# Optimization experiments

Measured on AMD Instinct MI355X. Metric: run time of the kernel, lower is better.

## Reference

```python
import math
import jax, jax.numpy as jnp
import numpy as np

NUM_HEADS = 8
C_HIDDEN = 32
C_Q = 64
C_KV = 64
INF = 1.0e9


def setup_inputs() -> dict:
    key = jax.random.key(0)
    ks = jax.random.split(key, 8)
    B, S, Q, KV = 1, 128, 256, 256
    H, D = NUM_HEADS, C_HIDDEN
    input_q = jax.random.normal(ks[0], (B, S, Q, C_Q), dtype=jnp.float32)
    input_kv = jax.random.normal(ks[1], (B, S, KV, C_KV), dtype=jnp.float32)
    mask = jnp.ones((B, S, 1, 1, KV), dtype=jnp.float32)
    bias = jax.random.normal(ks[2], (B, 1, H, Q, KV), dtype=jnp.float32)
    # Glorot-ish init for projections
    wq = jax.random.normal(ks[3], (C_Q, H * D), dtype=jnp.float32) * (1.0 / math.sqrt(C_Q))
    wk = jax.random.normal(ks[4], (C_KV, H * D), dtype=jnp.float32) * (1.0 / math.sqrt(C_KV))
    wv = jax.random.normal(ks[5], (C_KV, H * D), dtype=jnp.float32) * (1.0 / math.sqrt(C_KV))
    wo = jax.random.normal(ks[6], (H * D, C_Q), dtype=jnp.float32) * (1.0 / math.sqrt(H * D))
    bo = jnp.zeros((C_Q,), dtype=jnp.float32)
    return {"input_q": input_q, "input_kv": input_kv, "mask": mask, "bias": bias,
            "wq": wq, "wk": wk, "wv": wv, "wo": wo, "bo": bo}


def _split_heads(x):
    # [..., L, H*D] -> [..., H, L, D]
    *lead, L, HD = x.shape
    x = x.reshape(*lead, L, NUM_HEADS, C_HIDDEN)
    return jnp.swapaxes(x, -2, -3)


def reference(input_q, input_kv, mask, bias, wq, wk, wv, wo, bo):
    q = _split_heads(input_q @ wq)   # [B,S,H,Q,D]
    k = _split_heads(input_kv @ wk)  # [B,S,H,KV,D]
    v = _split_heads(input_kv @ wv)  # [B,S,H,KV,D]
    scaling = 1.0 / math.sqrt(C_HIDDEN)
    a = jnp.einsum("bshqd,bshkd->bshqk", q * scaling, k)
    a = a + (mask - 1.0) * INF + bias
    a = jax.nn.softmax(a, axis=-1)
    o = jnp.einsum("bshqk,bshkd->bshqd", a, v)
    o = jnp.swapaxes(o, -2, -3)  # [B,S,Q,H,D]
    o = o.reshape(o.shape[:-2] + (NUM_HEADS * C_HIDDEN,))
    return o @ wo + bo
```

## Files before the change

### kernel.cpp

```cpp
#include <hip/hip_runtime.h>

typedef __bf16 bf16_t;
typedef __bf16 bf16x4_t __attribute__((ext_vector_type(4)));
typedef __bf16 bf16x8 __attribute__((ext_vector_type(8)));
typedef float f32x4 __attribute__((ext_vector_type(4)));

#define NH 8
#define DH 32
#define QL 256
#define KL 256
#define CIN 64
#define HD 256

__device__ __forceinline__ bf16_t f2bf(float x) { return (bf16_t)x; }

__device__ __forceinline__ f32x4 mfma16(bf16x8 a, bf16x8 b, f32x4 c) {
    return __builtin_amdgcn_mfma_f32_16x16x32_bf16(a, b, c, 0, 0, 0);
}

__device__ __forceinline__ float exp2_raw(float x) {
    float r;
    asm("v_exp_f32 %0, %1" : "=v"(r) : "v"(x));
    return r;
}

__launch_bounds__(256)
__global__ void pack_w(const float* __restrict__ Wq, const float* __restrict__ Wk,
                       const float* __restrict__ Wv, const float* __restrict__ Wo,
                       bf16_t* __restrict__ WqF, bf16_t* __restrict__ WkF,
                       bf16_t* __restrict__ WvF, bf16_t* __restrict__ WoF) {
    const int h = blockIdx.x;
    const int tid = threadIdx.x, lane = tid & 63, w = tid >> 6;
    const int quad = lane >> 4, l16 = lane & 15;
    if (w < 3) {
        const float* __restrict__ W = (w == 0) ? Wq : (w == 1 ? Wk : Wv);
        bf16_t* __restrict__ F = (w == 0) ? WqF : (w == 1 ? WkF : WvF);
#pragma unroll
        for (int nt = 0; nt < 2; ++nt)
#pragma unroll
            for (int ks = 0; ks < 2; ++ks) {
                bf16x8 f;
#pragma unroll
                for (int j = 0; j < 8; ++j)
                    f[j] = f2bf(W[(ks * 32 + quad * 8 + j) * HD + h * DH + nt * 16 + l16]);
                *(bf16x8*)&F[(size_t)((h * 4 + nt * 2 + ks) * 512) + lane * 8] = f;
            }
    } else {
#pragma unroll
        for (int nt = 0; nt < 4; ++nt) {
            bf16x8 f;
#pragma unroll
            for (int j = 0; j < 8; ++j)
                f[j] = f2bf(Wo[(h * DH + (j >> 2) * 16 + quad * 4 + (j & 3)) * CIN +
                               nt * 16 + l16]);
            *(bf16x8*)&WoF[(size_t)((h * 4 + nt) * 512) + lane * 8] = f;
        }
    }
}

__launch_bounds__(256, 2)
__global__ void fused_pipe5(const float* __restrict__ Xq, const float* __restrict__ Xkv,
                            const float* __restrict__ Mask, const float* __restrict__ Bias,
                            const bf16_t* __restrict__ WqF, const bf16_t* __restrict__ WkF,
                            const bf16_t* __restrict__ WvF, const bf16_t* __restrict__ WoF,
                            const float* __restrict__ Bo, float* __restrict__ Out) {
    const int b = blockIdx.x;
    const int s = b & 127, qq = b >> 7;
    const int tid = threadIdx.x, lane = tid & 63, w = tid >> 6;
    const int quad = lane >> 4, l16 = lane & 15;
    const int tg = qq * 4 + w;
    const f32x4 vzero = {0.f, 0.f, 0.f, 0.f};
    constexpr float L2E = 1.4426950408889634f;

    __shared__ __attribute__((aligned(16))) bf16_t sK[2][KL * 40];
    __shared__ __attribute__((aligned(16))) bf16_t sVT[2][DH][264];
    __shared__ __attribute__((aligned(16))) float sMask[KL];

    if (tid < 64) {
        const f32x4 m4 = *(const f32x4*)&Mask[s * KL + tid * 4];
        f32x4 mm;
#pragma unroll
        for (int j = 0; j < 4; ++j) mm[j] = (m4[j] - 1.0f) * (1.0e9f * L2E);
        *(f32x4*)&sMask[tid * 4] = mm;
    }

    bf16x8 xk[4][2];
#pragma unroll
    for (int t = 0; t < 4; ++t) {
        const int row = (w * 4 + t) * 16 + l16;
        const float* src = &Xkv[(size_t)(s * QL + row) * CIN];
#pragma unroll
        for (int ks = 0; ks < 2; ++ks) {
            const f32x4 lo = *(const f32x4*)&src[ks * 32 + quad * 8];
            const f32x4 hi = *(const f32x4*)&src[ks * 32 + quad * 8 + 4];
            bf16x8 f;
#pragma unroll
            for (int j = 0; j < 4; ++j) { f[j] = f2bf(lo[j]); f[4 + j] = f2bf(hi[j]); }
            xk[t][ks] = f;
        }
    }
    bf16x8 xq[2];
    {
        const int row = tg * 16 + l16;
        const float* src = &Xq[(size_t)(s * QL + row) * CIN];
        const float qs = 0.17677669529663687f * L2E;
#pragma unroll
        for (int ks = 0; ks < 2; ++ks) {
            const f32x4 lo = *(const f32x4*)&src[ks * 32 + quad * 8];
            const f32x4 hi = *(const f32x4*)&src[ks * 32 + quad * 8 + 4];
            bf16x8 f;
#pragma unroll
            for (int j = 0; j < 4; ++j) {
                f[j] = f2bf(lo[j] * qs);
                f[4 + j] = f2bf(hi[j] * qs);
            }
            xq[ks] = f;
        }
    }

    auto projKV = [&](int h, int buf) {
        bf16x8 bk[2][2], bv[2][2];
#pragma unroll
        for (int nt = 0; nt < 2; ++nt)
#pragma unroll
            for (int ks = 0; ks < 2; ++ks) {
                bk[nt][ks] = *(const bf16x8*)&WkF[(size_t)((h * 4 + nt * 2 + ks) * 512) + lane * 8];
                bv[nt][ks] = *(const bf16x8*)&WvF[(size_t)((h * 4 + nt * 2 + ks) * 512) + lane * 8];
            }
#pragma unroll
        for (int t = 0; t < 4; ++t) {
            const int row = (w * 4 + t) * 16 + l16;
#pragma unroll
            for (int nt = 0; nt < 2; ++nt) {
                f32x4 c = mfma16(bk[nt][0], xk[t][0], vzero);
                c = mfma16(bk[nt][1], xk[t][1], c);
                bf16x4_t p4;
#pragma unroll
                for (int r = 0; r < 4; ++r) p4[r] = f2bf(c[r]);
                *(bf16x4_t*)&sK[buf][row * 40 + quad * 8 + nt * 4] = p4;
            }
        }
#pragma unroll
        for (int t = 0; t < 4; ++t) {
            const int c0 = (w * 4 + t) * 16 + quad * 4;
#pragma unroll
            for (int nt = 0; nt < 2; ++nt) {
                f32x4 c = mfma16(xk[t][0], bv[nt][0], vzero);
                c = mfma16(xk[t][1], bv[nt][1], c);
                bf16x4_t p4;
#pragma unroll
                for (int r = 0; r < 4; ++r) p4[r] = f2bf(c[r]);
                *(bf16x4_t*)&sVT[buf][nt * 16 + l16][c0] = p4;
            }
        }
    };
    auto projQ = [&](int h) -> bf16x8 {
        bf16x8 bq[2][2];
#pragma unroll
        for (int nt = 0; nt < 2; ++nt)
#pragma unroll
            for (int ks = 0; ks < 2; ++ks)
                bq[nt][ks] = *(const bf16x8*)&WqF[(size_t)((h * 4 + nt * 2 + ks) * 512) + lane * 8];
        bf16x8 q;
#pragma unroll
        for (int nt = 0; nt < 2; ++nt) {
            f32x4 c = mfma16(bq[nt][0], xq[0], vzero);
            c = mfma16(bq[nt][1], xq[1], c);
#pragma unroll
            for (int r = 0; r < 4; ++r) q[nt * 4 + r] = f2bf(c[r]);
        }
        return q;
    };

    auto loadVA = [&](int p, int c, bf16x8& v0, bf16x8& v1) {
        const bf16x4_t a00 = *(const bf16x4_t*)&sVT[p][l16][c * 32 + quad * 4];
        const bf16x4_t a01 = *(const bf16x4_t*)&sVT[p][l16][c * 32 + 16 + quad * 4];
        const bf16x4_t a10 = *(const bf16x4_t*)&sVT[p][16 + l16][c * 32 + quad * 4];
        const bf16x4_t a11 = *(const bf16x4_t*)&sVT[p][16 + l16][c * 32 + 16 + quad * 4];
#pragma unroll
        for (int j = 0; j < 4; ++j) {
            v0[j] = a00[j];
            v0[4 + j] = a01[j];
            v1[j] = a10[j];
            v1[4 + j] = a11[j];
        }
    };

    f32x4 acc[4];
#pragma unroll
    for (int nt = 0; nt < 4; ++nt) acc[nt] = vzero;

    f32x4 sv[16];
    {
        const float* bb = &Bias[(size_t)(tg * 16 + l16) * KL];
#pragma unroll
        for (int ct = 0; ct < 16; ++ct) sv[ct] = *(const f32x4*)&bb[ct * 16 + quad * 4];
    }
    projKV(0, 0);
    bf16x8 qfr = projQ(0);
    __syncthreads();
#pragma unroll
    for (int ct = 0; ct < 16; ++ct) {
        const f32x4 m4 = *(const f32x4*)&sMask[ct * 16 + quad * 4];
#pragma unroll
        for (int r = 0; r < 4; ++r) sv[ct][r] = sv[ct][r] * L2E + m4[r];
    }

#pragma unroll 1
    for (int h = 0; h < NH; ++h) {
        const int p = h & 1;
        const int hn = (h + 1) & 7;
        const float* bbn = &Bias[(size_t)(hn * QL + tg * 16 + l16) * KL];

#pragma unroll
        for (int ct = 0; ct < 16; ++ct) {
            const bf16x8 ak = *(const bf16x8*)&sK[p][(ct * 16 + l16) * 40 + quad * 8];
            sv[ct] = mfma16(ak, qfr, sv[ct]);
        }

        if (h + 1 < NH) projKV(h + 1, p ^ 1);

        bf16x8 bwo[4];
#pragma unroll
        for (int nt = 0; nt < 4; ++nt)
            bwo[nt] = *(const bf16x8*)&WoF[(size_t)((h * 4 + nt) * 512) + lane * 8];

        bf16x8 vc0, vc1;
        loadVA(p, 0, vc0, vc1);

        f32x4 vmx = sv[0];
#pragma unroll
        for (int ct = 1; ct < 16; ++ct)
#pragma unroll
            for (int r = 0; r < 4; ++r) vmx[r] = fmaxf(vmx[r], sv[ct][r]);
        float mx = fmaxf(fmaxf(vmx[0], vmx[1]), fmaxf(vmx[2], vmx[3]));
        mx = fmaxf(mx, __shfl_xor(mx, 16, 64));
        mx = fmaxf(mx, __shfl_xor(mx, 32, 64));
        f32x4 vsum = vzero;
#pragma unroll
        for (int ct = 0; ct < 16; ++ct)
#pragma unroll
            for (int r = 0; r < 4; ++r) {
                const float e = exp2_raw(sv[ct][r] - mx);
                sv[ct][r] = e;
                vsum[r] += e;
            }
        float sum = (vsum[0] + vsum[1]) + (vsum[2] + vsum[3]);
        sum += __shfl_xor(sum, 16, 64);
        sum += __shfl_xor(sum, 32, 64);
        const float rs = 1.0f / sum;

        f32x4 ot0 = vzero, ot1 = vzero;
#pragma unroll
        for (int c = 0; c < 8; ++c) {
            bf16x8 vn0, vn1;
            if (c < 7) loadVA(p, c + 1, vn0, vn1);
            bf16x8 pf;
#pragma unroll
            for (int j = 0; j < 4; ++j) {
                pf[j] = f2bf(sv[2 * c][j]);
                pf[4 + j] = f2bf(sv[2 * c + 1][j]);
            }
            sv[2 * c] = *(const f32x4*)&bbn[(2 * c) * 16 + quad * 4];
            sv[2 * c + 1] = *(const f32x4*)&bbn[(2 * c + 1) * 16 + quad * 4];
            ot0 = mfma16(vc0, pf, ot0);
            ot1 = mfma16(vc1, pf, ot1);
            vc0 = vn0;
            vc1 = vn1;
        }

        {
            bf16x8 af;
#pragma unroll
            for (int r = 0; r < 4; ++r) {
                af[r] = f2bf(ot0[r] * rs);
                af[4 + r] = f2bf(ot1[r] * rs);
            }
#pragma unroll
            for (int nt = 0; nt < 4; ++nt) acc[nt] = mfma16(af, bwo[nt], acc[nt]);
        }

        if (h + 1 < NH) {
            qfr = projQ(h + 1);
#pragma unroll
            for (int ct = 0; ct < 16; ++ct) {
                const f32x4 m4 = *(const f32x4*)&sMask[ct * 16 + quad * 4];
#pragma unroll
                for (int r = 0; r < 4; ++r) sv[ct][r] = sv[ct][r] * L2E + m4[r];
            }
        }

        __syncthreads();
    }

    const int orow = s * QL + tg * 16 + quad * 4;
#pragma unroll
    for (int nt = 0; nt < 4; ++nt) {
        const float bo = Bo[nt * 16 + l16];
#pragma unroll
        for (int r = 0; r < 4; ++r)
            Out[(size_t)(orow + r) * CIN + nt * 16 + l16] = acc[nt][r] + bo;
    }
}

extern "C" void kernel_launch(void* const* d_in, const int* in_sizes, int n_in,
                              void* d_out, int out_size, void* d_ws, size_t ws_size,
                              hipStream_t stream) {
    const float* Xq   = (const float*)d_in[0];
    const float* Xkv  = (const float*)d_in[1];
    const float* Mask = (const float*)d_in[2];
    const float* Bias = (const float*)d_in[3];
    const float* Wq   = (const float*)d_in[4];
    const float* Wk   = (const float*)d_in[5];
    const float* Wv   = (const float*)d_in[6];
    const float* Wo   = (const float*)d_in[7];
    const float* Bo   = (const float*)d_in[8];
    float* Out = (float*)d_out;

    bf16_t* WqF = (bf16_t*)d_ws;
    bf16_t* WkF = WqF + 16384;
    bf16_t* WvF = WkF + 16384;
    bf16_t* WoF = WvF + 16384;

    pack_w<<<dim3(NH), 256, 0, stream>>>(Wq, Wk, Wv, Wo, WqF, WkF, WvF, WoF);
    fused_pipe5<<<dim3(512), 256, 0, stream>>>(Xq, Xkv, Mask, Bias,
                                               WqF, WkF, WvF, WoF, Bo, Out);
}
```

Baseline: 135.2 us.

## Split each query tile's key range across two waves with cross-wave softmax reduction

```diff
diff --git a/kernel.cpp b/kernel.cpp
--- a/kernel.cpp
+++ b/kernel.cpp
@@ -58,23 +58,28 @@
     }
 }
 
-__launch_bounds__(256, 2)
-__global__ void fused_pipe5(const float* __restrict__ Xq, const float* __restrict__ Xkv,
-                            const float* __restrict__ Mask, const float* __restrict__ Bias,
-                            const bf16_t* __restrict__ WqF, const bf16_t* __restrict__ WkF,
-                            const bf16_t* __restrict__ WvF, const bf16_t* __restrict__ WoF,
-                            const float* __restrict__ Bo, float* __restrict__ Out) {
+__launch_bounds__(512, 4)
+__global__ void fused_w8(const float* __restrict__ Xq, const float* __restrict__ Xkv,
+                         const float* __restrict__ Mask, const float* __restrict__ Bias,
+                         const bf16_t* __restrict__ WqF, const bf16_t* __restrict__ WkF,
+                         const bf16_t* __restrict__ WvF, const bf16_t* __restrict__ WoF,
+                         const float* __restrict__ Bo, float* __restrict__ Out) {
     const int b = blockIdx.x;
     const int s = b & 127, qq = b >> 7;
     const int tid = threadIdx.x, lane = tid & 63, w = tid >> 6;
     const int quad = lane >> 4, l16 = lane & 15;
-    const int tg = qq * 4 + w;
+    const int wq = w & 3, hv = w >> 2;
+    const int tg = qq * 4 + wq;
+    const int ct0 = hv * 8;
+    const int cc0 = hv * 4;
     const f32x4 vzero = {0.f, 0.f, 0.f, 0.f};
     constexpr float L2E = 1.4426950408889634f;
 
     __shared__ __attribute__((aligned(16))) bf16_t sK[2][KL * 40];
     __shared__ __attribute__((aligned(16))) bf16_t sVT[2][DH][264];
     __shared__ __attribute__((aligned(16))) float sMask[KL];
+    __shared__ float sRed[8][16];
+    __shared__ float sSum[2][8][16];
 
     if (tid < 64) {
         const f32x4 m4 = *(const f32x4*)&Mask[s * KL + tid * 4];
@@ -84,10 +89,10 @@
         *(f32x4*)&sMask[tid * 4] = mm;
     }
 
-    bf16x8 xk[4][2];
-#pragma unroll
-    for (int t = 0; t < 4; ++t) {
-        const int row = (w * 4 + t) * 16 + l16;
+    bf16x8 xk[2][2];
+#pragma unroll
+    for (int t = 0; t < 2; ++t) {
+        const int row = (2 * w + t) * 16 + l16;
         const float* src = &Xkv[(size_t)(s * QL + row) * CIN];
 #pragma unroll
         for (int ks = 0; ks < 2; ++ks) {
@@ -128,8 +133,8 @@
                 bv[nt][ks] = *(const bf16x8*)&WvF[(size_t)((h * 4 + nt * 2 + ks) * 512) + lane * 8];
             }
 #pragma unroll
-        for (int t = 0; t < 4; ++t) {
-            const int row = (w * 4 + t) * 16 + l16;
+        for (int t = 0; t < 2; ++t) {
+            const int row = (2 * w + t) * 16 + l16;
 #pragma unroll
             for (int nt = 0; nt < 2; ++nt) {
                 f32x4 c = mfma16(bk[nt][0], xk[t][0], vzero);
@@ -141,8 +146,8 @@
             }
         }
 #pragma unroll
-        for (int t = 0; t < 4; ++t) {
-            const int c0 = (w * 4 + t) * 16 + quad * 4;
+        for (int t = 0; t < 2; ++t) {
+            const int c0v = (2 * w + t) * 16 + quad * 4;
 #pragma unroll
             for (int nt = 0; nt < 2; ++nt) {
                 f32x4 c = mfma16(xk[t][0], bv[nt][0], vzero);
@@ -150,7 +155,7 @@
                 bf16x4_t p4;
 #pragma unroll
                 for (int r = 0; r < 4; ++r) p4[r] = f2bf(c[r]);
-                *(bf16x4_t*)&sVT[buf][nt * 16 + l16][c0] = p4;
+                *(bf16x4_t*)&sVT[buf][nt * 16 + l16][c0v] = p4;
             }
         }
     };
@@ -171,7 +176,6 @@
         }
         return q;
     };
-
     auto loadVA = [&](int p, int c, bf16x8& v0, bf16x8& v1) {
         const bf16x4_t a00 = *(const bf16x4_t*)&sVT[p][l16][c * 32 + quad * 4];
         const bf16x4_t a01 = *(const bf16x4_t*)&sVT[p][l16][c * 32 + 16 + quad * 4];
@@ -189,117 +193,151 @@
     f32x4 acc[4];
 #pragma unroll
     for (int nt = 0; nt < 4; ++nt) acc[nt] = vzero;
-
-    f32x4 sv[16];
+    f32x4 ot0 = vzero, ot1 = vzero;
+    float psum = 0.f;
+    bf16x8 bwo[4];
+
+    f32x4 sv[8];
     {
         const float* bb = &Bias[(size_t)(tg * 16 + l16) * KL];
 #pragma unroll
-        for (int ct = 0; ct < 16; ++ct) sv[ct] = *(const f32x4*)&bb[ct * 16 + quad * 4];
+        for (int c = 0; c < 8; ++c)
+            sv[c] = *(const f32x4*)&bb[(ct0 + c) * 16 + quad * 4];
     }
     projKV(0, 0);
     bf16x8 qfr = projQ(0);
     __syncthreads();
 #pragma unroll
-    for (int ct = 0; ct < 16; ++ct) {
-        const f32x4 m4 = *(const f32x4*)&sMask[ct * 16 + quad * 4];
-#pragma unroll
-        for (int r = 0; r < 4; ++r) sv[ct][r] = sv[ct][r] * L2E + m4[r];
+    for (int c = 0; c < 8; ++c) {
+        const f32x4 m4 = *(const f32x4*)&sMask[(ct0 + c) * 16 + quad * 4];
+#pragma unroll
+        for (int r = 0; r < 4; ++r) sv[c][r] = sv[c][r] * L2E + m4[r];
     }
 
 #pragma unroll 1
     for (int h = 0; h < NH; ++h) {
         const int p = h & 1;
+
+        if (h > 0) {
+            const float rs = 1.0f / (psum + sSum[p ^ 1][w ^ 4][l16]);
+            bf16x8 af;
+#pragma unroll
+            for (int r = 0; r < 4; ++r) {
+                af[r] = f2bf(ot0[r] * rs);
+                af[4 + r] = f2bf(ot1[r] * rs);
+            }
+#pragma unroll
+            for (int nt = 0; nt < 4; ++nt) acc[nt] = mfma16(af, bwo[nt], acc[nt]);
+        }
+
+#pragma unroll
+        for (int c = 0; c < 8; ++c) {
+            const bf16x8 ak = *(const bf16x8*)&sK[p][((ct0 + c) * 16 + l16) * 40 + quad * 8];
+            sv[c] = mfma16(ak, qfr, sv[c]);
+        }
+        f32x4 vmx = sv[0];
+#pragma unroll
+        for (int c = 1; c < 8; ++c)
+#pragma unroll
+            for (int r = 0; r < 4; ++r) vmx[r] = fmaxf(vmx[r], sv[c][r]);
+        float pmax = fmaxf(fmaxf(vmx[0], vmx[1]), fmaxf(vmx[2], vmx[3]));
+        pmax = fmaxf(pmax, __shfl_xor(pmax, 16, 64));
+        pmax = fmaxf(pmax, __shfl_xor(pmax, 32, 64));
+        if (lane < 16) sRed[w][lane] = pmax;
+
+        __syncthreads();
+
+        const float gmax = fmaxf(pmax, sRed[w ^ 4][l16]);
+
+        if (h + 1 < NH) projKV(h + 1, p ^ 1);
+
+#pragma unroll
+        for (int nt = 0; nt < 4; ++nt)
+            bwo[nt] = *(const bf16x8*)&WoF[(size_t)((h * 4 + nt) * 512) + lane * 8];
+
+        f32x4 vsum = vzero;
+#pragma unroll
+        for (int c = 0; c < 8; ++c)
+#pragma unroll
+            for (int r = 0; r < 4; ++r) {
+                const float e = exp2_raw(sv[c][r] - gmax);
+                sv[c][r] = e;
+                vsum[r] += e;
+            }
+        float ps = (vsum[0] + vsum[1]) + (vsum[2] + vsum[3]);
+        ps += __shfl_xor(ps, 16, 64);
+        ps += __shfl_xor(ps, 32, 64);
+        psum = ps;
+        if (lane < 16) sSum[p][w][lane] = ps;
+
         const int hn = (h + 1) & 7;
         const float* bbn = &Bias[(size_t)(hn * QL + tg * 16 + l16) * KL];
-
-#pragma unroll
-        for (int ct = 0; ct < 16; ++ct) {
-            const bf16x8 ak = *(const bf16x8*)&sK[p][(ct * 16 + l16) * 40 + quad * 8];
-            sv[ct] = mfma16(ak, qfr, sv[ct]);
-        }
-
-        if (h + 1 < NH) projKV(h + 1, p ^ 1);
-
-        bf16x8 bwo[4];
-#pragma unroll
-        for (int nt = 0; nt < 4; ++nt)
-            bwo[nt] = *(const bf16x8*)&WoF[(size_t)((h * 4 + nt) * 512) + lane * 8];
-
         bf16x8 vc0, vc1;
-        loadVA(p, 0, vc0, vc1);
-
-        f32x4 vmx = sv[0];
-#pragma unroll
-        for (int ct = 1; ct < 16; ++ct)
-#pragma unroll
-            for (int r = 0; r < 4; ++r) vmx[r] = fmaxf(vmx[r], sv[ct][r]);
-        float mx = fmaxf(fmaxf(vmx[0], vmx[1]), fmaxf(vmx[2], vmx[3]));
-        mx = fmaxf(mx, __shfl_xor(mx, 16, 64));
-        mx = fmaxf(mx, __shfl_xor(mx, 32, 64));
-        f32x4 vsum = vzero;
-#pragma unroll
-        for (int ct = 0; ct < 16; ++ct)
-#pragma unroll
-            for (int r = 0; r < 4; ++r) {
-                const float e = exp2_raw(sv[ct][r] - mx);
-                sv[ct][r] = e;
-                vsum[r] += e;
-            }
-        float sum = (vsum[0] + vsum[1]) + (vsum[2] + vsum[3]);
-        sum += __shfl_xor(sum, 16, 64);
-        sum += __shfl_xor(sum, 32, 64);
-        const float rs = 1.0f / sum;
-
-        f32x4 ot0 = vzero, ot1 = vzero;
-#pragma unroll
-        for (int c = 0; c < 8; ++c) {
+        loadVA(p, cc0, vc0, vc1);
+        ot0 = vzero;
+        ot1 = vzero;
+#pragma unroll
+        for (int cl = 0; cl < 4; ++cl) {
             bf16x8 vn0, vn1;
-            if (c < 7) loadVA(p, c + 1, vn0, vn1);
+            if (cl < 3) loadVA(p, cc0 + cl + 1, vn0, vn1);
             bf16x8 pf;
 #pragma unroll
             for (int j = 0; j < 4; ++j) {
-                pf[j] = f2bf(sv[2 * c][j]);
-                pf[4 + j] = f2bf(sv[2 * c + 1][j]);
-            }
-            sv[2 * c] = *(const f32x4*)&bbn[(2 * c) * 16 + quad * 4];
-            sv[2 * c + 1] = *(const f32x4*)&bbn[(2 * c + 1) * 16 + quad * 4];
+                pf[j] = f2bf(sv[2 * cl][j]);
+                pf[4 + j] = f2bf(sv[2 * cl + 1][j]);
+            }
+            sv[2 * cl] = *(const f32x4*)&bbn[(ct0 + 2 * cl) * 16 + quad * 4];
+            sv[2 * cl + 1] = *(const f32x4*)&bbn[(ct0 + 2 * cl + 1) * 16 + quad * 4];
             ot0 = mfma16(vc0, pf, ot0);
             ot1 = mfma16(vc1, pf, ot1);
             vc0 = vn0;
             vc1 = vn1;
         }
 
-        {
-            bf16x8 af;
-#pragma unroll
-            for (int r = 0; r < 4; ++r) {
-                af[r] = f2bf(ot0[r] * rs);
-                af[4 + r] = f2bf(ot1[r] * rs);
-            }
-#pragma unroll
-            for (int nt = 0; nt < 4; ++nt) acc[nt] = mfma16(af, bwo[nt], acc[nt]);
-        }
-
         if (h + 1 < NH) {
             qfr = projQ(h + 1);
 #pragma unroll
-            for (int ct = 0; ct < 16; ++ct) {
-                const f32x4 m4 = *(const f32x4*)&sMask[ct * 16 + quad * 4];
-#pragma unroll
-                for (int r = 0; r < 4; ++r) sv[ct][r] = sv[ct][r] * L2E + m4[r];
+            for (int c = 0; c < 8; ++c) {
+                const f32x4 m4 = *(const f32x4*)&sMask[(ct0 + c) * 16 + quad * 4];
+#pragma unroll
+                for (int r = 0; r < 4; ++r) sv[c][r] = sv[c][r] * L2E + m4[r];
             }
         }
 
         __syncthreads();
     }
 
-    const int orow = s * QL + tg * 16 + quad * 4;
-#pragma unroll
-    for (int nt = 0; nt < 4; ++nt) {
-        const float bo = Bo[nt * 16 + l16];
-#pragma unroll
-        for (int r = 0; r < 4; ++r)
-            Out[(size_t)(orow + r) * CIN + nt * 16 + l16] = acc[nt][r] + bo;
+    {
+        const float rs = 1.0f / (psum + sSum[1][w ^ 4][l16]);
+        bf16x8 af;
+#pragma unroll
+        for (int r = 0; r < 4; ++r) {
+            af[r] = f2bf(ot0[r] * rs);
+            af[4 + r] = f2bf(ot1[r] * rs);
+        }
+#pragma unroll
+        for (int nt = 0; nt < 4; ++nt) acc[nt] = mfma16(af, bwo[nt], acc[nt]);
+    }
+    float* scr = (float*)&sK[0][0];
+    if (hv == 1) {
+#pragma unroll
+        for (int nt = 0; nt < 4; ++nt)
+#pragma unroll
+            for (int r = 0; r < 4; ++r)
+                scr[(wq * 64 + lane) * 16 + nt * 4 + r] = acc[nt][r];
+    }
+    __syncthreads();
+    if (hv == 0) {
+        const int orow = s * QL + tg * 16 + quad * 4;
+#pragma unroll
+        for (int nt = 0; nt < 4; ++nt) {
+            const float bo = Bo[nt * 16 + l16];
+#pragma unroll
+            for (int r = 0; r < 4; ++r) {
+                const float v = acc[nt][r] + scr[(wq * 64 + lane) * 16 + nt * 4 + r];
+                Out[(size_t)(orow + r) * CIN + nt * 16 + l16] = v + bo;
+            }
+        }
     }
 }
 
@@ -323,6 +361,6 @@
     bf16_t* WoF = WvF + 16384;
 
     pack_w<<<dim3(NH), 256, 0, stream>>>(Wq, Wk, Wv, Wo, WqF, WkF, WvF, WoF);
-    fused_pipe5<<<dim3(512), 256, 0, stream>>>(Xq, Xkv, Mask, Bias,
-                                               WqF, WkF, WvF, WoF, Bo, Out);
-}
+    fused_w8<<<dim3(512), 512, 0, stream>>>(Xq, Xkv, Mask, Bias,
+                                            WqF, WkF, WvF, WoF, Bo, Out);
+}
```

New measurement: 214.7 us. 58.8% more time.
